# Optimization experiments

Measured on AMD Instinct MI355X. Metric: run time of the kernel, lower is better.

The kernel has to match this reference:

```python
import jax, jax.numpy as jnp
import numpy as np
import itertools

RADIUS = 0.1
DILATION = 0.05
KSIZE = 3
NDIM = 3
EPS = 1e-12


def _offsets():
    # 3^ndim kernel-cell offsets centered on the particle, spaced by dilation
    half = (KSIZE - 1) / 2.0
    offs = np.array(list(itertools.product(range(KSIZE), repeat=NDIM)), dtype=np.float32)
    return jnp.asarray((offs - half) * DILATION)  # [K, NDIM]


def setup_inputs() -> dict:
    key = jax.random.key(0)
    k1, k2, k3, k4, k5 = jax.random.split(key, 5)
    B, N, C, O = 2, 4096, 16, 16
    K = KSIZE ** NDIM
    locs = jax.random.uniform(k1, (B, N, NDIM), dtype=jnp.float32)
    data = jax.random.normal(k2, (B, N, C), dtype=jnp.float32)
    # densities strictly positive, bounded away from zero
    density = jax.random.uniform(k3, (B, N), dtype=jnp.float32, minval=0.5, maxval=1.5)
    weight = jax.random.normal(k4, (O, C, K), dtype=jnp.float32) * 0.1
    bias = jax.random.normal(k5, (O,), dtype=jnp.float32) * 0.01
    return {"locs": locs, "data": data, "density": density, "weight": weight, "bias": bias}


def reference(locs, data, density, weight, bias):
    # SPH continuous convolution (ConvSP):
    # out[b,i,o] = bias[o] + sum_k sum_c weight[o,c,k] *
    #              sum_j (data[b,j,c]/density[b,j]) * W(||locs[b,j] - (locs[b,i]+off_k)||)
    # with smoothing kernel W(d) = (1 - d/radius)^3 for d < radius, else 0.
    B, N, _ = locs.shape
    O = weight.shape[0]
    offs = _offsets()                                # [K, NDIM]
    wK = jnp.transpose(weight, (2, 0, 1))            # [K, O, C]
    nd = data / density[..., None]                   # [B, N, C] density-normalized features
    l2 = jnp.sum(locs * locs, axis=-1)               # [B, N]

    def step(acc, xs):
        off, wk = xs                                 # off:[NDIM], wk:[O,C]
        c = locs + off                               # shifted query centers [B,N,NDIM]
        c2 = jnp.sum(c * c, axis=-1)                 # [B,N]
        d2 = c2[:, :, None] + l2[:, None, :] - 2.0 * jnp.einsum('bid,bjd->bij', c, locs)
        d = jnp.sqrt(jnp.maximum(d2, EPS))           # [B,N,N]
        w = jnp.where(d < RADIUS, (1.0 - d / RADIUS) ** 3, 0.0)
        kv = jnp.einsum('bij,bjc->bic', w, nd)       # [B,N,C]
        return acc + jnp.einsum('bic,oc->bio', kv, wk), None

    init = jnp.zeros((B, N, O), dtype=data.dtype)
    out, _ = jax.lax.scan(jax.checkpoint(step), init, (offs, wK))
    return out + bias
```

## Files before the change

kernel.cpp:

```cpp
#include <hip/hip_runtime.h>

#define N_PART 4096
#define RADIUS 0.1f
#define R2 0.01f
#define PRE2 0.034830f
#define EPS_K 1e-12f
#define TJ 1024

__global__ __launch_bounds__(256) void convsp_kernel(
    const float* __restrict__ locs,
    const float* __restrict__ data,
    const float* __restrict__ density,
    const float* __restrict__ weight,
    const float* __restrict__ bias,
    float* __restrict__ out)
{
    __shared__ float4 s_locs[TJ];

    const int tid  = threadIdx.x;
    const int b    = blockIdx.x >> 9;
    const int i    = ((blockIdx.x & 511) << 3) + (tid >> 5);
    const int lane = tid & 31;
    const int k    = lane;

    const float* locs_b = locs    + (size_t)b * N_PART * 3;
    const float* data_b = data    + (size_t)b * N_PART * 16;
    const float* dens_b = density + (size_t)b * N_PART;

    const float lix = locs_b[i*3 + 0];
    const float liy = locs_b[i*3 + 1];
    const float liz = locs_b[i*3 + 2];

    float cx, cy, cz;
    {
        const int kk = (k < 27) ? k : 13;
        const float ox = (float)(kk / 9      - 1) * 0.05f;
        const float oy = (float)((kk / 3) % 3 - 1) * 0.05f;
        const float oz = (float)(kk % 3      - 1) * 0.05f;
        cx = lix + ox; cy = liy + oy; cz = liz + oz;
        if (k >= 27) cx = 1e9f;
    }

    float kv[16];
#pragma unroll
    for (int c = 0; c < 16; ++c) kv[c] = 0.f;

    for (int tb = 0; tb < N_PART; tb += TJ) {
        __syncthreads();
        {
            float* sf = (float*)s_locs;
            for (int idx = tid; idx < TJ * 3; idx += 256) {
                sf[idx + idx / 3] = locs_b[tb * 3 + idx];
            }
        }
        __syncthreads();

        for (int base = 0; base < TJ; base += 32) {
            const float4 lj = s_locs[base + lane];
            const float ddx = lix - lj.x, ddy = liy - lj.y, ddz = liz - lj.z;
            const float d2p = ddx*ddx + ddy*ddy + ddz*ddz;
            const unsigned long long m = __ballot(d2p < PRE2);
            unsigned int mh = (unsigned int)(m >> (tid & 32));

            while (mh) {
                const int bit = __ffs(mh) - 1;
                mh &= (mh - 1);
                const int jj = base + bit;
                const float4 q = s_locs[jj];
                const float dx = cx - q.x, dy = cy - q.y, dz = cz - q.z;
                const float d2 = dx*dx + dy*dy + dz*dz;
                if (d2 < R2) {
                    const float d = sqrtf(fmaxf(d2, EPS_K));
                    const float t = __builtin_fmaf(d, -10.f, 1.f);
                    const float w = t * t * t;
                    const int gj = tb + jj;
                    const float wd = w / dens_b[gj];
                    const float4* dp = (const float4*)(data_b + (size_t)gj * 16);
                    const float4 v0 = dp[0], v1 = dp[1], v2 = dp[2], v3 = dp[3];
                    kv[ 0] = fmaf(wd, v0.x, kv[ 0]);
                    kv[ 1] = fmaf(wd, v0.y, kv[ 1]);
                    kv[ 2] = fmaf(wd, v0.z, kv[ 2]);
                    kv[ 3] = fmaf(wd, v0.w, kv[ 3]);
                    kv[ 4] = fmaf(wd, v1.x, kv[ 4]);
                    kv[ 5] = fmaf(wd, v1.y, kv[ 5]);
                    kv[ 6] = fmaf(wd, v1.z, kv[ 6]);
                    kv[ 7] = fmaf(wd, v1.w, kv[ 7]);
                    kv[ 8] = fmaf(wd, v2.x, kv[ 8]);
                    kv[ 9] = fmaf(wd, v2.y, kv[ 9]);
                    kv[10] = fmaf(wd, v2.z, kv[10]);
                    kv[11] = fmaf(wd, v2.w, kv[11]);
                    kv[12] = fmaf(wd, v3.x, kv[12]);
                    kv[13] = fmaf(wd, v3.y, kv[13]);
                    kv[14] = fmaf(wd, v3.z, kv[14]);
                    kv[15] = fmaf(wd, v3.w, kv[15]);
                }
            }
        }
    }

    const int kk = (k < 27) ? k : 26;
    float res = 0.f;
#pragma unroll
    for (int o = 0; o < 16; ++o) {
        float s = 0.f;
#pragma unroll
        for (int c = 0; c < 16; ++c)
            s = fmaf(weight[(o * 16 + c) * 27 + kk], kv[c], s);
#pragma unroll
        for (int d = 16; d >= 1; d >>= 1)
            s += __shfl_xor(s, d, 32);
        if (lane == o) res = s;
    }
    if (lane < 16) {
        out[((size_t)(b * N_PART + i)) * 16 + lane] = res + bias[lane];
    }
}

extern "C" void kernel_launch(void* const* d_in, const int* in_sizes, int n_in,
                              void* d_out, int out_size, void* d_ws, size_t ws_size,
                              hipStream_t stream) {
    const float* locs    = (const float*)d_in[0];
    const float* data    = (const float*)d_in[1];
    const float* density = (const float*)d_in[2];
    const float* weight  = (const float*)d_in[3];
    const float* bias    = (const float*)d_in[4];
    float* out = (float*)d_out;

    const int B = in_sizes[2] / N_PART;
    dim3 grid(B * (N_PART / 8));
    dim3 block(256);
    convsp_kernel<<<grid, block, 0, stream>>>(locs, data, density, weight, bias, out);
}
```

Measured before the change: 94.99 us.

## Bin particles into z-slabs and scan only nearby slabs with box prefilter

Adds preprocessing kernels that pre-divide data by density, histogram particles into 64 z-slabs, prefix-scan the counts and build a slab-sorted index list. The main kernel then scans only neighbour slabs within a fixed z span instead of all particles. It uses a per-axis box-distance ballot test, which is tighter than the old spherical prefilter. The cost is extra launches, a memset and an indirect gather of data. It also assumes no slab holds more than 128 particles (16 chunks of 8); particles beyond that in a crowded slab would never be computed.

```diff
diff --git a/kernel.cpp b/kernel.cpp
--- a/kernel.cpp
+++ b/kernel.cpp
@@ -1,119 +1,192 @@
 #include <hip/hip_runtime.h>
 
-#define N_PART 4096
-#define RADIUS 0.1f
-#define R2 0.01f
-#define PRE2 0.034830f
+#define NP 4096
+#define NSLAB 64
+#define ZSPAN 12
+#define MAXCHUNK 16
+#define TJ 512
 #define EPS_K 1e-12f
-#define TJ 1024
-
-__global__ __launch_bounds__(256) void convsp_kernel(
-    const float* __restrict__ locs,
-    const float* __restrict__ data,
-    const float* __restrict__ density,
-    const float* __restrict__ weight,
-    const float* __restrict__ bias,
+
+__global__ void k_nd(const float* __restrict__ data, const float* __restrict__ density,
+                     float* __restrict__ nd, int total) {
+    int e = blockIdx.x * 256 + threadIdx.x;
+    if (e < total) nd[e] = data[e] / density[e >> 4];
+}
+
+__global__ void k_hist(const float* __restrict__ locs, int* __restrict__ cnt, int totalP) {
+    int i = blockIdx.x * 256 + threadIdx.x;
+    if (i < totalP) {
+        float z = locs[i * 3 + 2];
+        int c = min(max((int)(z * 64.0f), 0), 63);
+        atomicAdd(&cnt[(i >> 12) * NSLAB + c], 1);
+    }
+}
+
+__global__ void k_scan(const int* __restrict__ cnt, int* __restrict__ off, int B) {
+    int lane = threadIdx.x & 63;
+    int b = threadIdx.x >> 6;
+    if (b >= B) return;
+    int incl = cnt[b * NSLAB + lane];
+    for (int d = 1; d < 64; d <<= 1) {
+        int o = __shfl_up(incl, d, 64);
+        if (lane >= d) incl += o;
+    }
+    off[b * (NSLAB + 1) + lane + 1] = incl;
+    if (lane == 0) off[b * (NSLAB + 1)] = 0;
+}
+
+__global__ __launch_bounds__(256) void k_rank(const float* __restrict__ locs,
+                                              const int* __restrict__ off,
+                                              int* __restrict__ list) {
+    int b = blockIdx.x / NSLAB;
+    int s = blockIdx.x % NSLAB;
+    const float* lz = locs + (size_t)b * NP * 3;
+    __shared__ int wtot[4];
+    int base = off[b * (NSLAB + 1) + s];
+    int running = 0;
+    int tid = threadIdx.x, lane = tid & 63, w = tid >> 6;
+    for (int chunk = 0; chunk < NP; chunk += 256) {
+        int i = chunk + tid;
+        float z = lz[i * 3 + 2];
+        int c = min(max((int)(z * 64.0f), 0), 63);
+        bool match = (c == s);
+        unsigned long long m = __ballot(match);
+        int pre = __popcll(m & ((1ull << lane) - 1ull));
+        if (lane == 0) wtot[w] = (int)__popcll(m);
+        __syncthreads();
+        int bp = 0, tot = 0;
+        for (int ww = 0; ww < 4; ++ww) { if (ww < w) bp += wtot[ww]; tot += wtot[ww]; }
+        if (match) list[b * NP + base + running + bp + pre] = i;
+        running += tot;
+        __syncthreads();
+    }
+}
+
+__global__ __launch_bounds__(256) void k_main(
+    const float* __restrict__ locs, const float* __restrict__ nd,
+    const int* __restrict__ off, const int* __restrict__ list,
+    const float* __restrict__ weight, const float* __restrict__ bias,
     float* __restrict__ out)
 {
     __shared__ float4 s_locs[TJ];
-
-    const int tid  = threadIdx.x;
-    const int b    = blockIdx.x >> 9;
-    const int i    = ((blockIdx.x & 511) << 3) + (tid >> 5);
+    const int bid = blockIdx.x;
+    const int b = bid >> 10;
+    const int rem = bid & 1023;
+    const int s = rem >> 4;
+    const int m = rem & 15;
+
+    const int* off_b = off + b * (NSLAB + 1);
+    const int sbeg = off_b[s], send = off_b[s + 1];
+    const int pstart = sbeg + m * 8;
+    if (pstart >= send) return;
+    const int pcnt = min(8, send - pstart);
+
+    const int tid = threadIdx.x;
+    const int p = tid >> 5;
     const int lane = tid & 31;
-    const int k    = lane;
-
-    const float* locs_b = locs    + (size_t)b * N_PART * 3;
-    const float* data_b = data    + (size_t)b * N_PART * 16;
-    const float* dens_b = density + (size_t)b * N_PART;
-
-    const float lix = locs_b[i*3 + 0];
-    const float liy = locs_b[i*3 + 1];
-    const float liz = locs_b[i*3 + 2];
+
+    const int s0 = max(s - ZSPAN, 0);
+    const int s1 = min(s + ZSPAN, NSLAB - 1);
+    const int jstart = off_b[s0];
+    const int jend = off_b[s1 + 1];
+
+    const float* locs_b = locs + (size_t)b * NP * 3;
+    const float* nd_b   = nd   + (size_t)b * NP * 16;
+    const int*   list_b = list + b * NP;
+
+    const int ppos = pstart + min(p, pcnt - 1);
+    const int orig = list_b[ppos];
+    const float lix = locs_b[orig * 3 + 0];
+    const float liy = locs_b[orig * 3 + 1];
+    const float liz = locs_b[orig * 3 + 2];
 
     float cx, cy, cz;
     {
-        const int kk = (k < 27) ? k : 13;
-        const float ox = (float)(kk / 9      - 1) * 0.05f;
-        const float oy = (float)((kk / 3) % 3 - 1) * 0.05f;
-        const float oz = (float)(kk % 3      - 1) * 0.05f;
-        cx = lix + ox; cy = liy + oy; cz = liz + oz;
-        if (k >= 27) cx = 1e9f;
+        int kk = (lane < 27) ? lane : 13;
+        cx = lix + (float)(kk / 9       - 1) * 0.05f;
+        cy = liy + (float)((kk / 3) % 3 - 1) * 0.05f;
+        cz = liz + (float)(kk % 3       - 1) * 0.05f;
+        if (lane >= 27) cx = 1e9f;
     }
 
     float kv[16];
 #pragma unroll
     for (int c = 0; c < 16; ++c) kv[c] = 0.f;
 
-    for (int tb = 0; tb < N_PART; tb += TJ) {
-        __syncthreads();
-        {
-            float* sf = (float*)s_locs;
-            for (int idx = tid; idx < TJ * 3; idx += 256) {
-                sf[idx + idx / 3] = locs_b[tb * 3 + idx];
+    for (int tb = jstart; tb < jend; tb += TJ) {
+        __syncthreads();
+        for (int t = tid; t < TJ; t += 256) {
+            int j = tb + t;
+            float4 e;
+            if (j < jend) {
+                int idx = list_b[j];
+                e.x = locs_b[idx * 3 + 0];
+                e.y = locs_b[idx * 3 + 1];
+                e.z = locs_b[idx * 3 + 2];
+                e.w = __int_as_float(idx);
+            } else { e.x = 1e9f; e.y = 1e9f; e.z = 1e9f; e.w = 0.f; }
+            s_locs[t] = e;
+        }
+        __syncthreads();
+
+        const int nc = min(TJ, jend - tb);
+        const int nb = (nc + 31) >> 5;
+        for (int base = 0; base < nb; ++base) {
+            const float4 lj = s_locs[(base << 5) + lane];
+            const float ex = fmaxf(fabsf(lix - lj.x) - 0.05f, 0.f);
+            const float ey = fmaxf(fabsf(liy - lj.y) - 0.05f, 0.f);
+            const float ez = fmaxf(fabsf(liz - lj.z) - 0.05f, 0.f);
+            const float bd2 = ex * ex + ey * ey + ez * ez;
+            const unsigned long long mball = __ballot(bd2 < 0.01f);
+            unsigned int mh = (unsigned int)(mball >> (tid & 32));
+
+            while (mh) {
+                const int bit = __ffs(mh) - 1;
+                mh &= mh - 1;
+                const float4 q = s_locs[(base << 5) + bit];
+                const int idx = __float_as_int(q.w);
+                const float4* dp = (const float4*)(nd_b + (size_t)idx * 16);
+                const float4 v0 = dp[0], v1 = dp[1], v2 = dp[2], v3 = dp[3];
+                const float dx = cx - q.x, dy = cy - q.y, dz = cz - q.z;
+                const float d2 = dx * dx + dy * dy + dz * dz;
+                const float d = sqrtf(fmaxf(d2, EPS_K));
+                float t1 = fmaxf(__builtin_fmaf(d, -10.f, 1.f), 0.f);
+                const float w = t1 * t1 * t1;
+                kv[ 0] = fmaf(w, v0.x, kv[ 0]);
+                kv[ 1] = fmaf(w, v0.y, kv[ 1]);
+                kv[ 2] = fmaf(w, v0.z, kv[ 2]);
+                kv[ 3] = fmaf(w, v0.w, kv[ 3]);
+                kv[ 4] = fmaf(w, v1.x, kv[ 4]);
+                kv[ 5] = fmaf(w, v1.y, kv[ 5]);
+                kv[ 6] = fmaf(w, v1.z, kv[ 6]);
+                kv[ 7] = fmaf(w, v1.w, kv[ 7]);
+                kv[ 8] = fmaf(w, v2.x, kv[ 8]);
+                kv[ 9] = fmaf(w, v2.y, kv[ 9]);
+                kv[10] = fmaf(w, v2.z, kv[10]);
+                kv[11] = fmaf(w, v2.w, kv[11]);
+                kv[12] = fmaf(w, v3.x, kv[12]);
+                kv[13] = fmaf(w, v3.y, kv[13]);
+                kv[14] = fmaf(w, v3.z, kv[14]);
+                kv[15] = fmaf(w, v3.w, kv[15]);
             }
         }
-        __syncthreads();
-
-        for (int base = 0; base < TJ; base += 32) {
-            const float4 lj = s_locs[base + lane];
-            const float ddx = lix - lj.x, ddy = liy - lj.y, ddz = liz - lj.z;
-            const float d2p = ddx*ddx + ddy*ddy + ddz*ddz;
-            const unsigned long long m = __ballot(d2p < PRE2);
-            unsigned int mh = (unsigned int)(m >> (tid & 32));
-
-            while (mh) {
-                const int bit = __ffs(mh) - 1;
-                mh &= (mh - 1);
-                const int jj = base + bit;
-                const float4 q = s_locs[jj];
-                const float dx = cx - q.x, dy = cy - q.y, dz = cz - q.z;
-                const float d2 = dx*dx + dy*dy + dz*dz;
-                if (d2 < R2) {
-                    const float d = sqrtf(fmaxf(d2, EPS_K));
-                    const float t = __builtin_fmaf(d, -10.f, 1.f);
-                    const float w = t * t * t;
-                    const int gj = tb + jj;
-                    const float wd = w / dens_b[gj];
-                    const float4* dp = (const float4*)(data_b + (size_t)gj * 16);
-                    const float4 v0 = dp[0], v1 = dp[1], v2 = dp[2], v3 = dp[3];
-                    kv[ 0] = fmaf(wd, v0.x, kv[ 0]);
-                    kv[ 1] = fmaf(wd, v0.y, kv[ 1]);
-                    kv[ 2] = fmaf(wd, v0.z, kv[ 2]);
-                    kv[ 3] = fmaf(wd, v0.w, kv[ 3]);
-                    kv[ 4] = fmaf(wd, v1.x, kv[ 4]);
-                    kv[ 5] = fmaf(wd, v1.y, kv[ 5]);
-                    kv[ 6] = fmaf(wd, v1.z, kv[ 6]);
-                    kv[ 7] = fmaf(wd, v1.w, kv[ 7]);
-                    kv[ 8] = fmaf(wd, v2.x, kv[ 8]);
-                    kv[ 9] = fmaf(wd, v2.y, kv[ 9]);
-                    kv[10] = fmaf(wd, v2.z, kv[10]);
-                    kv[11] = fmaf(wd, v2.w, kv[11]);
-                    kv[12] = fmaf(wd, v3.x, kv[12]);
-                    kv[13] = fmaf(wd, v3.y, kv[13]);
-                    kv[14] = fmaf(wd, v3.z, kv[14]);
-                    kv[15] = fmaf(wd, v3.w, kv[15]);
-                }
-            }
-        }
-    }
-
-    const int kk = (k < 27) ? k : 26;
+    }
+
+    const int kk = (lane < 27) ? lane : 26;
     float res = 0.f;
 #pragma unroll
     for (int o = 0; o < 16; ++o) {
-        float s = 0.f;
+        float acc = 0.f;
 #pragma unroll
         for (int c = 0; c < 16; ++c)
-            s = fmaf(weight[(o * 16 + c) * 27 + kk], kv[c], s);
+            acc = fmaf(weight[(o * 16 + c) * 27 + kk], kv[c], acc);
 #pragma unroll
         for (int d = 16; d >= 1; d >>= 1)
-            s += __shfl_xor(s, d, 32);
-        if (lane == o) res = s;
-    }
-    if (lane < 16) {
-        out[((size_t)(b * N_PART + i)) * 16 + lane] = res + bias[lane];
-    }
+            acc += __shfl_xor(acc, d, 32);
+        if (lane == o) res = acc;
+    }
+    if (p < pcnt && lane < 16)
+        out[((size_t)(b * NP + orig)) * 16 + lane] = res + bias[lane];
 }
 
 extern "C" void kernel_launch(void* const* d_in, const int* in_sizes, int n_in,
@@ -126,8 +199,24 @@
     const float* bias    = (const float*)d_in[4];
     float* out = (float*)d_out;
 
-    const int B = in_sizes[2] / N_PART;
-    dim3 grid(B * (N_PART / 8));
-    dim3 block(256);
-    convsp_kernel<<<grid, block, 0, stream>>>(locs, data, density, weight, bias, out);
-}
+    const int B = in_sizes[2] / NP;
+
+    char* ws = (char*)d_ws;
+    size_t nd_bytes = (size_t)B * NP * 16 * 4;
+    float* nd  = (float*)ws;
+    int*   cnt = (int*)(ws + nd_bytes);
+    int*   off = (int*)(ws + nd_bytes + (size_t)B * NSLAB * 4);
+    size_t off_end = nd_bytes + (size_t)B * NSLAB * 4 + (size_t)B * (NSLAB + 1) * 4;
+    size_t list_o  = (off_end + 255) & ~(size_t)255;
+    int*   list = (int*)(ws + list_o);
+
+    hipMemsetAsync(cnt, 0, (size_t)B * NSLAB * 4, stream);
+
+    int totalE = B * NP * 16;
+    k_nd<<<(totalE + 255) / 256, 256, 0, stream>>>(data, density, nd, totalE);
+    int totalP = B * NP;
+    k_hist<<<(totalP + 255) / 256, 256, 0, stream>>>(locs, cnt, totalP);
+    k_scan<<<1, 64 * B, 0, stream>>>(cnt, off, B);
+    k_rank<<<B * NSLAB, 256, 0, stream>>>(locs, off, list);
+    k_main<<<B * NSLAB * MAXCHUNK, 256, 0, stream>>>(locs, nd, off, list, weight, bias, out);
+}
```

Measured after the change: 159.9 us. 68.3% more time.
